# Kernel optimization log

Measured on AMD Instinct MI355X. Metric: run time of the kernel, lower is better.

## Reference

```python
import jax, jax.numpy as jnp
import numpy as np

EMBED_DIM = 384
NUM_HEADS = 6
HEAD_DIM = EMBED_DIM // NUM_HEADS
MLP_HIDDEN = 4 * EMBED_DIM
LN_EPS = 1e-5


def layer_norm(x, gamma, beta):
    mu = jnp.mean(x, axis=-1, keepdims=True)
    var = jnp.mean((x - mu) ** 2, axis=-1, keepdims=True)
    return (x - mu) * jax.lax.rsqrt(var + LN_EPS) * gamma + beta


def setup_inputs() -> dict:
    key = jax.random.key(0)
    ks = jax.random.split(key, 8)
    D, H = EMBED_DIM, MLP_HIDDEN
    s = 1.0 / np.sqrt(D)
    sh = 1.0 / np.sqrt(H)
    return {
        "x": jax.random.normal(ks[0], (16, 1024, D), dtype=jnp.float32),
        "ln1_g": jnp.ones((D,), jnp.float32),
        "ln1_b": jnp.zeros((D,), jnp.float32),
        "qkv_w": jax.random.uniform(ks[1], (3 * D, D), jnp.float32, -s, s),
        "qkv_b": jax.random.uniform(ks[2], (3 * D,), jnp.float32, -s, s),
        "proj_w": jax.random.uniform(ks[3], (D, D), jnp.float32, -s, s),
        "proj_b": jax.random.uniform(ks[4], (D,), jnp.float32, -s, s),
        "ln2_g": jnp.ones((D,), jnp.float32),
        "ln2_b": jnp.zeros((D,), jnp.float32),
        "fc1_w": jax.random.uniform(ks[5], (H, D), jnp.float32, -s, s),
        "fc1_b": jax.random.uniform(ks[6], (H,), jnp.float32, -s, s),
        "fc2_w": jax.random.uniform(ks[7], (D, H), jnp.float32, -sh, sh),
        "fc2_b": jnp.zeros((D,), jnp.float32),
    }


def reference(x, ln1_g, ln1_b, qkv_w, qkv_b, proj_w, proj_b,
              ln2_g, ln2_b, fc1_w, fc1_b, fc2_w, fc2_b):
    B, N, D = x.shape
    Hh, Dh = NUM_HEADS, HEAD_DIM
    scale = Dh ** -0.5

    # --- attention sublayer (pre-norm) ---
    h = layer_norm(x, ln1_g, ln1_b)
    qkv = h @ qkv_w.T + qkv_b                      # [B,N,3D]
    qkv = qkv.reshape(B, N, 3, Hh, Dh)
    q, k, v = (qkv[:, :, i].transpose(0, 2, 1, 3) for i in range(3))  # [B,H,N,Dh]
    attn = jax.nn.softmax(jnp.einsum('bhnd,bhmd->bhnm', q, k) * scale, axis=-1)
    o = jnp.einsum('bhnm,bhmd->bhnd', attn, v)     # [B,H,N,Dh]
    o = o.transpose(0, 2, 1, 3).reshape(B, N, D)
    x = x + (o @ proj_w.T + proj_b)

    # --- MLP sublayer (pre-norm) ---
    h = layer_norm(x, ln2_g, ln2_b)
    h = jax.nn.gelu(h @ fc1_w.T + fc1_b, approximate=False)
    x = x + (h @ fc2_w.T + fc2_b)
    return x
```

## Files before the change

kernel.cpp:

```cpp
#include <hip/hip_runtime.h>

typedef unsigned short u16;
typedef unsigned int   u32;
typedef __bf16  bf16x8 __attribute__((ext_vector_type(8)));
typedef __bf16  bf16x4_t __attribute__((ext_vector_type(4)));
typedef float   f32x4  __attribute__((ext_vector_type(4)));
typedef float   f32x2  __attribute__((ext_vector_type(2)));

struct Ptrs { const void* p[13]; };

extern "C" __device__ float __ocml_native_exp2_f32(float);

__device__ __forceinline__ float bf2f(u16 u) {
    union { unsigned int i; float f; } c; c.i = ((unsigned int)u) << 16; return c.f;
}
__device__ __forceinline__ u16 f2bf(float f) {
    union { float f; unsigned int i; } c; c.f = f;
    unsigned int u = c.i;
    unsigned int r = (u + 0x7fffu + ((u >> 16) & 1u)) >> 16;
    return (u16)r;
}

__device__ __forceinline__ float wave_sum(float x) {
#pragma unroll
    for (int m = 32; m >= 1; m >>= 1) x += __shfl_xor(x, m);
    return x;
}

__device__ __forceinline__ void g2l16(const u16* g, u16* l) {
    __builtin_amdgcn_global_load_lds(
        (__attribute__((address_space(1))) void*)g,
        (__attribute__((address_space(3))) void*)l, 16, 0, 0);
}

__device__ __forceinline__ int sniff_bf16(const u32* __restrict__ w) {
    int cnt = 0;
    for (int i = 0; i < 128; ++i) {
        u16 lo = (u16)(w[i] & 0xFFFFu);
        int e = (lo >> 7) & 0xFF;
        cnt += (e >= 117 && e <= 123) ? 1 : 0;
    }
    return (cnt >= 64) ? 1 : 0;
}

__global__ __launch_bounds__(256) void k_convert(Ptrs ps,
                                                 u16* __restrict__ cw,
                                                 int* __restrict__ flagp)
{
    const int cum[13] = {0,48,96,55392,55536,73968,74016,74064,74112,
                         147840,148032,221760,221808};
    const int off[12] = {0,384,768,443136,444288,591744,
                         592128,592512,592896,1182720,1184256,1774080};
    const int flag = sniff_bf16((const u32*)ps.p[3]);
    if (blockIdx.x == 0 && threadIdx.x == 0) *flagp = flag;
    int c = blockIdx.x * 256 + threadIdx.x;
    if (c >= 221808) return;
    int seg = 0;
#pragma unroll
    for (int i = 1; i < 12; ++i) seg += (c >= cum[i]) ? 1 : 0;
    int e = (c - cum[seg]) * 8;
    u16* dst = cw + off[seg] + e;
    if (flag) {
        *(uint4*)dst = *((const uint4*)ps.p[seg + 1] + (e >> 3));
    } else {
        const float* s = (const float*)ps.p[seg + 1] + e;
        u16 tmp[8];
#pragma unroll
        for (int t = 0; t < 8; ++t) tmp[t] = f2bf(s[t]);
        *(uint4*)dst = *(const uint4*)tmp;
    }
}

__global__ __launch_bounds__(256) void k_ln1cvt(const void* __restrict__ xin,
                                                const u16* __restrict__ g,
                                                const u16* __restrict__ b,
                                                u16* __restrict__ cx,
                                                u16* __restrict__ h,
                                                const int* __restrict__ flagp)
{
    const int wid = threadIdx.x >> 6, lane = threadIdx.x & 63;
    const int row = blockIdx.x * 4 + wid;
    const int e0 = lane * 6;
    float v[6]; u16 raw[6];
    if (*flagp) {
        const u16* p = (const u16*)xin + (size_t)row * 384 + e0;
        u32 w0 = *(const u32*)(p);
        u32 w1 = *(const u32*)(p + 2);
        u32 w2 = *(const u32*)(p + 4);
        raw[0] = (u16)w0; raw[1] = (u16)(w0 >> 16);
        raw[2] = (u16)w1; raw[3] = (u16)(w1 >> 16);
        raw[4] = (u16)w2; raw[5] = (u16)(w2 >> 16);
#pragma unroll
        for (int t = 0; t < 6; t++) v[t] = bf2f(raw[t]);
    } else {
        const float* p = (const float*)xin + (size_t)row * 384 + e0;
        f32x2 a0 = *(const f32x2*)(p);
        f32x2 a1 = *(const f32x2*)(p + 2);
        f32x2 a2 = *(const f32x2*)(p + 4);
        v[0] = a0[0]; v[1] = a0[1]; v[2] = a1[0];
        v[3] = a1[1]; v[4] = a2[0]; v[5] = a2[1];
#pragma unroll
        for (int t = 0; t < 6; t++) raw[t] = f2bf(v[t]);
    }
    u32* pc = (u32*)(cx + (size_t)row * 384 + e0);
    pc[0] = (u32)raw[0] | ((u32)raw[1] << 16);
    pc[1] = (u32)raw[2] | ((u32)raw[3] << 16);
    pc[2] = (u32)raw[4] | ((u32)raw[5] << 16);
    float s = 0.f;
#pragma unroll
    for (int t = 0; t < 6; t++) s += v[t];
    const float mu = wave_sum(s) * (1.0f / 384.0f);
    float vs = 0.f;
#pragma unroll
    for (int t = 0; t < 6; t++) { float d = v[t] - mu; vs += d * d; }
    const float var = wave_sum(vs) * (1.0f / 384.0f);
    const float rs = rsqrtf(var + 1e-5f);
    const u32* gg = (const u32*)(g + e0);
    const u32* bb = (const u32*)(b + e0);
    u32 gw[3] = {gg[0], gg[1], gg[2]};
    u32 bw[3] = {bb[0], bb[1], bb[2]};
    u16 ow[6];
#pragma unroll
    for (int t = 0; t < 6; t++) {
        u16 ge = (u16)(gw[t >> 1] >> ((t & 1) * 16));
        u16 be = (u16)(bw[t >> 1] >> ((t & 1) * 16));
        ow[t] = f2bf((v[t] - mu) * rs * bf2f(ge) + bf2f(be));
    }
    u32* po = (u32*)(h + (size_t)row * 384 + e0);
    po[0] = (u32)ow[0] | ((u32)ow[1] << 16);
    po[1] = (u32)ow[2] | ((u32)ow[3] << 16);
    po[2] = (u32)ow[4] | ((u32)ow[5] << 16);
}

__device__ __forceinline__ void gemm_core_128(const u16* __restrict__ A,
                                              const u16* __restrict__ B,
                                              int K, int m0, int n0,
                                              f32x4 (&acc)[4][4])
{
    __shared__ __align__(16) u16 As[128 * 64];
    __shared__ __align__(16) u16 Bs[128 * 64];

    const int tid  = threadIdx.x;
    const int lane = tid & 63;
    const int wid  = tid >> 6;
    const int wm  = (wid >> 1) * 64;
    const int wn  = (wid & 1) * 64;
    const int l15 = lane & 15;
    const int g   = lane >> 4;
    const int srow   = lane >> 3;
    const int schunk = ((lane & 7) ^ srow) * 8;

    const u16* Abase = A + (size_t)(m0 + wid * 32 + srow) * K + schunk;
    const u16* Bbase = B + (size_t)(n0 + wid * 32 + srow) * K + schunk;

    for (int kk = 0; kk < K; kk += 64) {
        __syncthreads();
#pragma unroll
        for (int t = 0; t < 4; ++t) {
            g2l16(Abase + (size_t)t * 8 * K + kk, &As[(wid * 32 + t * 8) * 64]);
            g2l16(Bbase + (size_t)t * 8 * K + kk, &Bs[(wid * 32 + t * 8) * 64]);
        }
        __syncthreads();

#pragma unroll
        for (int ks = 0; ks < 2; ++ks) {
            bf16x8 af[4], bfr[4];
#pragma unroll
            for (int i = 0; i < 4; i++) {
                int row = wm + 16 * i + l15;
                int p = ((ks * 4 + g) ^ (l15 & 7)) * 8;
                af[i] = __builtin_bit_cast(bf16x8,
                         *(const uint4*)&As[row * 64 + p]);
            }
#pragma unroll
            for (int j = 0; j < 4; j++) {
                int row = wn + 16 * j + l15;
                int p = ((ks * 4 + g) ^ (l15 & 7)) * 8;
                bfr[j] = __builtin_bit_cast(bf16x8,
                         *(const uint4*)&Bs[row * 64 + p]);
            }
#pragma unroll
            for (int i = 0; i < 4; i++)
#pragma unroll
                for (int j = 0; j < 4; j++)
                    acc[i][j] = __builtin_amdgcn_mfma_f32_16x16x32_bf16(
                                    af[i], bfr[j], acc[i][j], 0, 0, 0);
        }
    }
}

__device__ __forceinline__ void gemm_core_128x64(const u16* __restrict__ A,
                                                 const u16* __restrict__ B,
                                                 int K, int m0, int n0,
                                                 f32x4 (&acc)[4][2])
{
    __shared__ __align__(16) u16 As[128 * 64];
    __shared__ __align__(16) u16 Bs[64 * 64];

    const int tid  = threadIdx.x;
    const int lane = tid & 63;
    const int wid  = tid >> 6;
    const int wm  = (wid >> 1) * 64;
    const int wn  = (wid & 1) * 32;
    const int l15 = lane & 15;
    const int g   = lane >> 4;
    const int srow   = lane >> 3;
    const int schunk = ((lane & 7) ^ srow) * 8;

    const u16* Abase = A + (size_t)(m0 + wid * 32 + srow) * K + schunk;
    const u16* Bbase = B + (size_t)(n0 + wid * 16 + srow) * K + schunk;

    for (int kk = 0; kk < K; kk += 64) {
        __syncthreads();
#pragma unroll
        for (int t = 0; t < 4; ++t)
            g2l16(Abase + (size_t)t * 8 * K + kk, &As[(wid * 32 + t * 8) * 64]);
#pragma unroll
        for (int t = 0; t < 2; ++t)
            g2l16(Bbase + (size_t)t * 8 * K + kk, &Bs[(wid * 16 + t * 8) * 64]);
        __syncthreads();

#pragma unroll
        for (int ks = 0; ks < 2; ++ks) {
            bf16x8 af[4], bfr[2];
#pragma unroll
            for (int i = 0; i < 4; i++) {
                int row = wm + 16 * i + l15;
                int p = ((ks * 4 + g) ^ (l15 & 7)) * 8;
                af[i] = __builtin_bit_cast(bf16x8,
                         *(const uint4*)&As[row * 64 + p]);
            }
#pragma unroll
            for (int j = 0; j < 2; j++) {
                int row = wn + 16 * j + l15;
                int p = ((ks * 4 + g) ^ (l15 & 7)) * 8;
                bfr[j] = __builtin_bit_cast(bf16x8,
                         *(const uint4*)&Bs[row * 64 + p]);
            }
#pragma unroll
            for (int i = 0; i < 4; i++)
#pragma unroll
                for (int j = 0; j < 2; j++)
                    acc[i][j] = __builtin_amdgcn_mfma_f32_16x16x32_bf16(
                                    af[i], bfr[j], acc[i][j], 0, 0, 0);
        }
    }
}

__global__ __launch_bounds__(256) void k_layernorm(const u16* __restrict__ in,
                                                   const u16* __restrict__ g,
                                                   const u16* __restrict__ b,
                                                   u16* __restrict__ out,
                                                   int nrows)
{
    const int wid = threadIdx.x >> 6, lane = threadIdx.x & 63;
    const int row = blockIdx.x * 4 + wid;
    if (row >= nrows) return;
    const int e0 = lane * 6;
    float v[6];
    const u16* p = in + (size_t)row * 384 + e0;
    u32 w0 = *(const u32*)(p);
    u32 w1 = *(const u32*)(p + 2);
    u32 w2 = *(const u32*)(p + 4);
    v[0] = bf2f((u16)w0); v[1] = bf2f((u16)(w0 >> 16));
    v[2] = bf2f((u16)w1); v[3] = bf2f((u16)(w1 >> 16));
    v[4] = bf2f((u16)w2); v[5] = bf2f((u16)(w2 >> 16));
    float s = 0.f;
#pragma unroll
    for (int t = 0; t < 6; t++) s += v[t];
    const float mu = wave_sum(s) * (1.0f / 384.0f);
    float vs = 0.f;
#pragma unroll
    for (int t = 0; t < 6; t++) { float d = v[t] - mu; vs += d * d; }
    const float var = wave_sum(vs) * (1.0f / 384.0f);
    const float rs = rsqrtf(var + 1e-5f);
    const u32* gg = (const u32*)(g + e0);
    const u32* bb = (const u32*)(b + e0);
    u32 gw[3] = {gg[0], gg[1], gg[2]};
    u32 bw[3] = {bb[0], bb[1], bb[2]};
    u16 ow[6];
#pragma unroll
    for (int t = 0; t < 6; t++) {
        u16 ge = (u16)(gw[t >> 1] >> ((t & 1) * 16));
        u16 be = (u16)(bw[t >> 1] >> ((t & 1) * 16));
        ow[t] = f2bf((v[t] - mu) * rs * bf2f(ge) + bf2f(be));
    }
    u32* po = (u32*)(out + (size_t)row * 384 + e0);
    po[0] = (u32)ow[0] | ((u32)ow[1] << 16);
    po[1] = (u32)ow[2] | ((u32)ow[3] << 16);
    po[2] = (u32)ow[4] | ((u32)ow[5] << 16);
}

__global__ __launch_bounds__(256) void k_gemm_qkv(const u16* __restrict__ A,
                                                  const u16* __restrict__ W,
                                                  const u16* __restrict__ bias,
                                                  u16* __restrict__ q,
                                                  u16* __restrict__ kbuf,
                                                  u16* __restrict__ vT)
{
    const int id = blockIdx.x, slot = id & 7, idx = id >> 3;
    const int m0 = (slot * 16 + idx / 9) * 128;
    const int n0 = (idx % 9) * 128;
    f32x4 acc[4][4];
#pragma unroll
    for (int i = 0; i < 4; i++)
#pragma unroll
        for (int j = 0; j < 4; j++) acc[i][j] = f32x4{0.f, 0.f, 0.f, 0.f};
    gemm_core_128(A, W, 384, m0, n0, acc);
    const int lane = threadIdx.x & 63, wid = threadIdx.x >> 6;
    const int wm = (wid >> 1) * 64, wn = (wid & 1) * 64;
    const int l15 = lane & 15, rq = (lane >> 4) * 4;
#pragma unroll
    for (int i = 0; i < 4; i++) {
        const int grb = m0 + wm + 16 * i + rq;
        const int bb = grb >> 10, nn = grb & 1023;
#pragma unroll
        for (int j = 0; j < 4; j++) {
            const int gc = n0 + wn + 16 * j + l15;
            const int part = gc / 384, rem = gc % 384;
            const int head = rem >> 6, dh = rem & 63;
            const int bh = bb * 6 + head;
            float vals[4];
#pragma unroll
            for (int r = 0; r < 4; r++) vals[r] = acc[i][j][r] + bf2f(bias[gc]);
            if (part == 2) {
                u32 lo = (u32)f2bf(vals[0]) | ((u32)f2bf(vals[1]) << 16);
                u32 hi = (u32)f2bf(vals[2]) | ((u32)f2bf(vals[3]) << 16);
                uint2 pk; pk.x = lo; pk.y = hi;
                *(uint2*)&vT[((size_t)bh * 64 + dh) * 1024 + nn] = pk;
            } else {
                u16* dst = part ? kbuf : q;
#pragma unroll
                for (int r = 0; r < 4; r++)
                    dst[((size_t)bh * 1024 + nn + r) * 64 + dh] = f2bf(vals[r]);
            }
        }
    }
}

__global__ __launch_bounds__(256) void k_attn(const u16* __restrict__ q,
                                              const u16* __restrict__ kk,
                                              const u16* __restrict__ vT,
                                              u16* __restrict__ o)
{
    __shared__ __align__(16) u16 Ks[128 * 64];
    __shared__ __align__(16) u16 Vs[2][64 * 64];
    __shared__ __align__(16) u16 Ps[128 * 64];

    const int tid = threadIdx.x, lane = tid & 63, wid = tid >> 6;
    const int l15 = lane & 15, g = lane >> 4, q8 = g * 8;
    const int id = blockIdx.x;
    const int bh = (id & 7) * 12 + ((id >> 3) >> 3);
    const int q0 = ((id >> 3) & 7) * 128;
    const int wrow = wid * 32;

    const u16* Q = q  + (size_t)bh * 65536;
    const u16* K = kk + (size_t)bh * 65536;
    const u16* V = vT + (size_t)bh * 65536;

    const int srow   = lane >> 3;
    const int schunk = ((lane & 7) ^ srow) * 8;
    const int rd0 = ((0 + g) ^ (l15 & 7)) * 8;
    const int rd1 = ((4 + g) ^ (l15 & 7)) * 8;
    int pcol[4];
#pragma unroll
    for (int ip = 0; ip < 4; ++ip)
        pcol[ip] = (((ip * 2 + (g >> 1)) ^ (l15 & 7)) * 8) + (g & 1) * 4;

    bf16x8 aq[2][2];
#pragma unroll
    for (int jp = 0; jp < 2; ++jp)
#pragma unroll
        for (int ks = 0; ks < 2; ++ks) {
            bf16x8 t = __builtin_bit_cast(bf16x8,
                *(const uint4*)&Q[(size_t)(q0 + wrow + jp * 16 + l15) * 64
                                  + ks * 32 + q8]);
#pragma unroll
            for (int e = 0; e < 8; ++e)
                t[e] = (__bf16)((float)t[e] * 0.18033688f);
            aq[jp][ks] = t;
        }

    f32x4 ob[2][4];
#pragma unroll
    for (int i = 0; i < 2; ++i)
#pragma unroll
        for (int j = 0; j < 4; ++j) ob[i][j] = f32x4{0.f, 0.f, 0.f, 0.f};
    float lsum[2] = {0.f, 0.f};

    for (int kt2 = 0; kt2 < 8; ++kt2) {
        __syncthreads();
#pragma unroll
        for (int t = 0; t < 4; ++t) {
            int r0 = wid * 32 + t * 8;
            g2l16(&K[(size_t)(kt2 * 128 + r0 + srow) * 64 + schunk], &Ks[r0 * 64]);
        }
#pragma unroll
        for (int h = 0; h < 2; ++h)
#pragma unroll
            for (int t = 0; t < 2; ++t) {
                int r0 = wid * 16 + t * 8;
                g2l16(&V[(size_t)(r0 + srow) * 1024 + kt2 * 128 + h * 64 + schunk],
                      &Vs[h][r0 * 64]);
            }
        __syncthreads();

#pragma unroll 1
        for (int h = 0; h < 2; ++h) {
            f32x4 st[4][2];
#pragma unroll
            for (int ip = 0; ip < 4; ++ip)
#pragma unroll
                for (int jp = 0; jp < 2; ++jp) st[ip][jp] = f32x4{0.f,0.f,0.f,0.f};
            __builtin_amdgcn_s_setprio(1);
#pragma unroll
            for (int ip = 0; ip < 4; ++ip) {
                int rbase = (h * 64 + ip * 16 + l15) * 64;
                bf16x8 bk0 = __builtin_bit_cast(bf16x8,
                    *(const uint4*)&Ks[rbase + rd0]);
                bf16x8 bk1 = __builtin_bit_cast(bf16x8,
                    *(const uint4*)&Ks[rbase + rd1]);
#pragma unroll
                for (int jp = 0; jp < 2; ++jp) {
                    st[ip][jp] = __builtin_amdgcn_mfma_f32_16x16x32_bf16(
                                    bk0, aq[jp][0], st[ip][jp], 0, 0, 0);
                    st[ip][jp] = __builtin_amdgcn_mfma_f32_16x16x32_bf16(
                                    bk1, aq[jp][1], st[ip][jp], 0, 0, 0);
                }
            }
            __builtin_amdgcn_s_setprio(0);

#pragma unroll
            for (int jp = 0; jp < 2; ++jp) {
                float ps = 0.f;
#pragma unroll
                for (int ip = 0; ip < 4; ++ip)
#pragma unroll
                    for (int r = 0; r < 4; ++r) {
                        float p = __ocml_native_exp2_f32(st[ip][jp][r]);
                        st[ip][jp][r] = p;
                        ps += p;
                    }
                lsum[jp] += ps;
            }

#pragma unroll
            for (int ip = 0; ip < 4; ++ip)
#pragma unroll
                for (int jp = 0; jp < 2; ++jp) {
                    bf16x4_t pk;
#pragma unroll
                    for (int r = 0; r < 4; ++r) pk[r] = (__bf16)st[ip][jp][r];
                    *(bf16x4_t*)&Ps[(wrow + jp*16 + l15) * 64 + pcol[ip]] = pk;
                }

            __builtin_amdgcn_s_setprio(1);
#pragma unroll
            for (int ks = 0; ks < 2; ++ks) {
                const int rdo = ks ? rd1 : rd0;
                bf16x8 ap[2];
#pragma unroll
                for (int i = 0; i < 2; ++i)
                    ap[i] = __builtin_bit_cast(bf16x8,
                        *(const uint4*)&Ps[(wrow + i*16 + l15) * 64 + rdo]);
#pragma unroll
                for (int jv = 0; jv < 4; ++jv) {
                    bf16x8 bv = __builtin_bit_cast(bf16x8,
                        *(const uint4*)&Vs[h][(jv * 16 + l15) * 64 + rdo]);
#pragma unroll
                    for (int i = 0; i < 2; ++i)
                        ob[i][jv] = __builtin_amdgcn_mfma_f32_16x16x32_bf16(
                                      ap[i], bv, ob[i][jv], 0, 0, 0);
                }
            }
            __builtin_amdgcn_s_setprio(0);
        }
    }

#pragma unroll
    for (int jp = 0; jp < 2; ++jp) {
        lsum[jp] += __shfl_xor(lsum[jp], 16);
        lsum[jp] += __shfl_xor(lsum[jp], 32);
    }
    const int bb = bh / 6, hh = bh % 6;
#pragma unroll
    for (int i = 0; i < 2; ++i)
#pragma unroll
        for (int r = 0; r < 4; ++r) {
            int src = (lane & 48) | (g * 4 + r);
            float linv = 1.0f / __shfl(lsum[i], src);
            int row = q0 + wrow + i * 16 + g * 4 + r;
#pragma unroll
            for (int jv = 0; jv < 4; ++jv) {
                int dh = jv * 16 + l15;
                o[((size_t)(bb * 1024 + row)) * 384 + hh * 64 + dh] =
                    f2bf(ob[i][jv][r] * linv);
            }
        }
}

__global__ __launch_bounds__(256) void k_gemm_proj(const u16* __restrict__ A,
                                                   const u16* __restrict__ W,
                                                   const u16* __restrict__ bias,
                                                   const u16* __restrict__ xin,
                                                   u16* __restrict__ x1)
{
    const int id = blockIdx.x, slot = id & 7, idx = id >> 3;
    const int m0 = (slot * 16 + idx / 6) * 128;
    const int n0 = (idx % 6) * 64;
    f32x4 acc[4][2];
#pragma unroll
    for (int i = 0; i < 4; i++)
#pragma unroll
        for (int j = 0; j < 2; j++) acc[i][j] = f32x4{0.f, 0.f, 0.f, 0.f};
    gemm_core_128x64(A, W, 384, m0, n0, acc);
    const int lane = threadIdx.x & 63, wid = threadIdx.x >> 6;
    const int wm = (wid >> 1) * 64, wn = (wid & 1) * 32;
    const int l15 = lane & 15, rq = (lane >> 4) * 4;
#pragma unroll
    for (int i = 0; i < 4; i++)
#pragma unroll
        for (int j = 0; j < 2; j++)
#pragma unroll
            for (int r = 0; r < 4; r++) {
                int gr = m0 + wm + 16 * i + rq + r;
                int gc = n0 + wn + 16 * j + l15;
                size_t ix = (size_t)gr * 384 + gc;
                x1[ix] = f2bf(acc[i][j][r] + bf2f(bias[gc]) + bf2f(xin[ix]));
            }
}

__global__ __launch_bounds__(256) void k_gemm_fc1(const u16* __restrict__ A,
                                                  const u16* __restrict__ W,
                                                  const u16* __restrict__ bias,
                                                  u16* __restrict__ hmid)
{
    const int id = blockIdx.x, slot = id & 7, idx = id >> 3;
    const int mbase = (slot * 8 + idx / 12) * 256;
    const int n0 = (idx % 12) * 128;
#pragma unroll 1
    for (int sub = 0; sub < 2; ++sub) {
        const int m0 = mbase + sub * 128;
        f32x4 acc[4][4];
#pragma unroll
        for (int i = 0; i < 4; i++)
#pragma unroll
            for (int j = 0; j < 4; j++) acc[i][j] = f32x4{0.f, 0.f, 0.f, 0.f};
        gemm_core_128(A, W, 384, m0, n0, acc);
        const int lane = threadIdx.x & 63, wid = threadIdx.x >> 6;
        const int wm = (wid >> 1) * 64, wn = (wid & 1) * 64;
        const int l15 = lane & 15, rq = (lane >> 4) * 4;
#pragma unroll
        for (int i = 0; i < 4; i++)
#pragma unroll
            for (int j = 0; j < 4; j++)
#pragma unroll
                for (int r = 0; r < 4; r++) {
                    int gr = m0 + wm + 16 * i + rq + r;
                    int gc = n0 + wn + 16 * j + l15;
                    float v = acc[i][j][r] + bf2f(bias[gc]);
                    float u = v * (1.5957691f + 0.0713548f * v * v);
                    float ge = v * __builtin_amdgcn_rcpf(1.0f + __expf(-u));
                    hmid[(size_t)gr * 1536 + gc] = f2bf(ge);
                }
    }
}

__global__ __launch_bounds__(256) void k_gemm_fc2(const u16* __restrict__ A,
                                                  const u16* __restrict__ W,
                                                  const u16* __restrict__ bias,
                                                  const u16* __restrict__ x1,
                                                  void* __restrict__ outv,
                                                  const int* __restrict__ flagp)
{
    const int id = blockIdx.x, slot = id & 7, idx = id >> 3;
    const int m0 = (slot * 16 + idx / 6) * 128;
    const int n0 = (idx % 6) * 64;
    f32x4 acc[4][2];
#pragma unroll
    for (int i = 0; i < 4; i++)
#pragma unroll
        for (int j = 0; j < 2; j++) acc[i][j] = f32x4{0.f, 0.f, 0.f, 0.f};
    gemm_core_128x64(A, W, 1536, m0, n0, acc);
    const int lane = threadIdx.x & 63, wid = threadIdx.x >> 6;
    const int wm = (wid >> 1) * 64, wn = (wid & 1) * 32;
    const int l15 = lane & 15, rq = (lane >> 4) * 4;
    const int isbf = *flagp;
    u16*   ob = (u16*)outv;
    float* of = (float*)outv;
#pragma unroll
    for (int i = 0; i < 4; i++)
#pragma unroll
        for (int j = 0; j < 2; j++)
#pragma unroll
            for (int r = 0; r < 4; r++) {
                int gr = m0 + wm + 16 * i + rq + r;
                int gc = n0 + wn + 16 * j + l15;
                size_t ix = (size_t)gr * 384 + gc;
                float v = acc[i][j][r] + bf2f(bias[gc]) + bf2f(x1[ix]);
                if (isbf) ob[ix] = f2bf(v);
                else      of[ix] = v;
            }
}

extern "C" void kernel_launch(void* const* d_in, const int* in_sizes, int n_in,
                              void* d_out, int out_size, void* d_ws, size_t ws_size,
                              hipStream_t stream)
{
    char* ws = (char*)d_ws;
    u16*   cw   = (u16*)(ws + 0);
    int*   flag = (int*)(ws + 3548928);
    u16*   cx   = (u16*)(ws + 3549184);
    u16*   h    = (u16*)(ws + 16132096);
    u16*   x1   = (u16*)(ws + 28715008);
    u16*   q    = (u16*)(ws + 53880832);
    u16*   kbuf = (u16*)(ws + 66463744);
    u16*   vT   = (u16*)(ws + 79046656);
    u16*   o    = (u16*)(ws + 91629568);
    u16*   hmid = (u16*)(ws + 53880832);

    const u16* c_ln1_g  = cw + 0;
    const u16* c_ln1_b  = cw + 384;
    const u16* c_qkv_w  = cw + 768;
    const u16* c_qkv_b  = cw + 443136;
    const u16* c_proj_w = cw + 444288;
    const u16* c_proj_b = cw + 591744;
    const u16* c_ln2_g  = cw + 592128;
    const u16* c_ln2_b  = cw + 592512;
    const u16* c_fc1_w  = cw + 592896;
    const u16* c_fc1_b  = cw + 1182720;
    const u16* c_fc2_w  = cw + 1184256;
    const u16* c_fc2_b  = cw + 1774080;

    Ptrs ps;
    for (int i = 0; i < 13; ++i) ps.p[i] = d_in[i];

    k_convert<<<867, 256, 0, stream>>>(ps, cw, flag);
    k_ln1cvt<<<4096, 256, 0, stream>>>(d_in[0], c_ln1_g, c_ln1_b, cx, h, flag);
    k_gemm_qkv<<<1152, 256, 0, stream>>>(h, c_qkv_w, c_qkv_b, q, kbuf, vT);
    k_attn<<<768, 256, 0, stream>>>(q, kbuf, vT, o);
    k_gemm_proj<<<768, 256, 0, stream>>>(o, c_proj_w, c_proj_b, cx, x1);
    k_layernorm<<<4096, 256, 0, stream>>>(x1, c_ln2_g, c_ln2_b, h, 16384);
    k_gemm_fc1<<<768, 256, 0, stream>>>(h, c_fc1_w, c_fc1_b, hmid);
    k_gemm_fc2<<<768, 256, 0, stream>>>(hmid, c_fc2_w, c_fc2_b, x1,
                                        d_out, flag);
    (void)in_sizes; (void)n_in; (void)out_size; (void)ws_size; (void)c_fc2_b;
}
```

Before: 268.2 us.

## Fuse weight conversion with LN1, swap QKV MFMA operands, use exp2 GELU

Merges the weight-conversion kernel and the LN1/convert kernel into one launch, with the LN1 blocks reading gamma and beta straight from the original inputs. The bf16 sniff loop is cut from 128 to 32 samples. The QKV GEMM swaps its MFMA operands so each lane holds consecutive head-dim values, which lets q and k be written as packed 8-byte stores while vT now gets scalar stores. The GELU epilogue folds the log2(e) factor into its constants and calls native exp2. Together these aim to remove one launch and cut store and transcendental overhead, at the cost of uncoalesced vT writes and a less robust dtype sniff.

```diff
diff --git a/kernel.cpp b/kernel.cpp
--- a/kernel.cpp
+++ b/kernel.cpp
@@ -35,55 +35,54 @@
 
 __device__ __forceinline__ int sniff_bf16(const u32* __restrict__ w) {
     int cnt = 0;
-    for (int i = 0; i < 128; ++i) {
+    for (int i = 0; i < 32; ++i) {
         u16 lo = (u16)(w[i] & 0xFFFFu);
         int e = (lo >> 7) & 0xFF;
         cnt += (e >= 117 && e <= 123) ? 1 : 0;
     }
-    return (cnt >= 64) ? 1 : 0;
-}
-
-__global__ __launch_bounds__(256) void k_convert(Ptrs ps,
+    return (cnt >= 16) ? 1 : 0;
+}
+
+__global__ __launch_bounds__(256) void k_cvt_ln1(Ptrs ps,
                                                  u16* __restrict__ cw,
-                                                 int* __restrict__ flagp)
-{
-    const int cum[13] = {0,48,96,55392,55536,73968,74016,74064,74112,
-                         147840,148032,221760,221808};
-    const int off[12] = {0,384,768,443136,444288,591744,
-                         592128,592512,592896,1182720,1184256,1774080};
+                                                 int* __restrict__ flagp,
+                                                 u16* __restrict__ cx,
+                                                 u16* __restrict__ h)
+{
     const int flag = sniff_bf16((const u32*)ps.p[3]);
     if (blockIdx.x == 0 && threadIdx.x == 0) *flagp = flag;
-    int c = blockIdx.x * 256 + threadIdx.x;
-    if (c >= 221808) return;
-    int seg = 0;
-#pragma unroll
-    for (int i = 1; i < 12; ++i) seg += (c >= cum[i]) ? 1 : 0;
-    int e = (c - cum[seg]) * 8;
-    u16* dst = cw + off[seg] + e;
-    if (flag) {
-        *(uint4*)dst = *((const uint4*)ps.p[seg + 1] + (e >> 3));
-    } else {
-        const float* s = (const float*)ps.p[seg + 1] + e;
-        u16 tmp[8];
-#pragma unroll
-        for (int t = 0; t < 8; ++t) tmp[t] = f2bf(s[t]);
-        *(uint4*)dst = *(const uint4*)tmp;
-    }
-}
-
-__global__ __launch_bounds__(256) void k_ln1cvt(const void* __restrict__ xin,
-                                                const u16* __restrict__ g,
-                                                const u16* __restrict__ b,
-                                                u16* __restrict__ cx,
-                                                u16* __restrict__ h,
-                                                const int* __restrict__ flagp)
-{
+
+    if (blockIdx.x < 867) {
+        const int cum[13] = {0,48,96,55392,55536,73968,74016,74064,74112,
+                             147840,148032,221760,221808};
+        const int off[12] = {0,384,768,443136,444288,591744,
+                             592128,592512,592896,1182720,1184256,1774080};
+        int c = blockIdx.x * 256 + threadIdx.x;
+        if (c >= 221808) return;
+        int seg = 0;
+#pragma unroll
+        for (int i = 1; i < 12; ++i) seg += (c >= cum[i]) ? 1 : 0;
+        int e = (c - cum[seg]) * 8;
+        u16* dst = cw + off[seg] + e;
+        if (flag) {
+            *(uint4*)dst = *((const uint4*)ps.p[seg + 1] + (e >> 3));
+        } else {
+            const float* s = (const float*)ps.p[seg + 1] + e;
+            u16 tmp[8];
+#pragma unroll
+            for (int t = 0; t < 8; ++t) tmp[t] = f2bf(s[t]);
+            *(uint4*)dst = *(const uint4*)tmp;
+        }
+        return;
+    }
+
     const int wid = threadIdx.x >> 6, lane = threadIdx.x & 63;
-    const int row = blockIdx.x * 4 + wid;
+    const int row = (blockIdx.x - 867) * 4 + wid;
     const int e0 = lane * 6;
     float v[6]; u16 raw[6];
-    if (*flagp) {
-        const u16* p = (const u16*)xin + (size_t)row * 384 + e0;
+    float gv[6], bv[6];
+    if (flag) {
+        const u16* p = (const u16*)ps.p[0] + (size_t)row * 384 + e0;
         u32 w0 = *(const u32*)(p);
         u32 w1 = *(const u32*)(p + 2);
         u32 w2 = *(const u32*)(p + 4);
@@ -92,8 +91,12 @@
         raw[4] = (u16)w2; raw[5] = (u16)(w2 >> 16);
 #pragma unroll
         for (int t = 0; t < 6; t++) v[t] = bf2f(raw[t]);
+        const u16* gp = (const u16*)ps.p[1] + e0;
+        const u16* bp = (const u16*)ps.p[2] + e0;
+#pragma unroll
+        for (int t = 0; t < 6; t++) { gv[t] = bf2f(gp[t]); bv[t] = bf2f(bp[t]); }
     } else {
-        const float* p = (const float*)xin + (size_t)row * 384 + e0;
+        const float* p = (const float*)ps.p[0] + (size_t)row * 384 + e0;
         f32x2 a0 = *(const f32x2*)(p);
         f32x2 a1 = *(const f32x2*)(p + 2);
         f32x2 a2 = *(const f32x2*)(p + 4);
@@ -101,6 +104,10 @@
         v[3] = a1[1]; v[4] = a2[0]; v[5] = a2[1];
 #pragma unroll
         for (int t = 0; t < 6; t++) raw[t] = f2bf(v[t]);
+        const float* gp = (const float*)ps.p[1] + e0;
+        const float* bp = (const float*)ps.p[2] + e0;
+#pragma unroll
+        for (int t = 0; t < 6; t++) { gv[t] = gp[t]; bv[t] = bp[t]; }
     }
     u32* pc = (u32*)(cx + (size_t)row * 384 + e0);
     pc[0] = (u32)raw[0] | ((u32)raw[1] << 16);
@@ -115,23 +122,17 @@
     for (int t = 0; t < 6; t++) { float d = v[t] - mu; vs += d * d; }
     const float var = wave_sum(vs) * (1.0f / 384.0f);
     const float rs = rsqrtf(var + 1e-5f);
-    const u32* gg = (const u32*)(g + e0);
-    const u32* bb = (const u32*)(b + e0);
-    u32 gw[3] = {gg[0], gg[1], gg[2]};
-    u32 bw[3] = {bb[0], bb[1], bb[2]};
     u16 ow[6];
 #pragma unroll
-    for (int t = 0; t < 6; t++) {
-        u16 ge = (u16)(gw[t >> 1] >> ((t & 1) * 16));
-        u16 be = (u16)(bw[t >> 1] >> ((t & 1) * 16));
-        ow[t] = f2bf((v[t] - mu) * rs * bf2f(ge) + bf2f(be));
-    }
+    for (int t = 0; t < 6; t++)
+        ow[t] = f2bf((v[t] - mu) * rs * gv[t] + bv[t]);
     u32* po = (u32*)(h + (size_t)row * 384 + e0);
     po[0] = (u32)ow[0] | ((u32)ow[1] << 16);
     po[1] = (u32)ow[2] | ((u32)ow[3] << 16);
     po[2] = (u32)ow[4] | ((u32)ow[5] << 16);
 }
 
+template <bool SWAP = false>
 __device__ __forceinline__ void gemm_core_128(const u16* __restrict__ A,
                                               const u16* __restrict__ B,
                                               int K, int m0, int n0,
@@ -182,9 +183,14 @@
 #pragma unroll
             for (int i = 0; i < 4; i++)
 #pragma unroll
-                for (int j = 0; j < 4; j++)
-                    acc[i][j] = __builtin_amdgcn_mfma_f32_16x16x32_bf16(
-                                    af[i], bfr[j], acc[i][j], 0, 0, 0);
+                for (int j = 0; j < 4; j++) {
+                    if (SWAP)
+                        acc[i][j] = __builtin_amdgcn_mfma_f32_16x16x32_bf16(
+                                        bfr[j], af[i], acc[i][j], 0, 0, 0);
+                    else
+                        acc[i][j] = __builtin_amdgcn_mfma_f32_16x16x32_bf16(
+                                        af[i], bfr[j], acc[i][j], 0, 0, 0);
+                }
         }
     }
 }
@@ -306,33 +312,33 @@
     for (int i = 0; i < 4; i++)
 #pragma unroll
         for (int j = 0; j < 4; j++) acc[i][j] = f32x4{0.f, 0.f, 0.f, 0.f};
-    gemm_core_128(A, W, 384, m0, n0, acc);
+    gemm_core_128<true>(A, W, 384, m0, n0, acc);
     const int lane = threadIdx.x & 63, wid = threadIdx.x >> 6;
     const int wm = (wid >> 1) * 64, wn = (wid & 1) * 64;
     const int l15 = lane & 15, rq = (lane >> 4) * 4;
 #pragma unroll
     for (int i = 0; i < 4; i++) {
-        const int grb = m0 + wm + 16 * i + rq;
-        const int bb = grb >> 10, nn = grb & 1023;
+        const int gr = m0 + wm + 16 * i + l15;
+        const int bb = gr >> 10, nn = gr & 1023;
 #pragma unroll
         for (int j = 0; j < 4; j++) {
-            const int gc = n0 + wn + 16 * j + l15;
-            const int part = gc / 384, rem = gc % 384;
-            const int head = rem >> 6, dh = rem & 63;
+            const int gcb = n0 + wn + 16 * j + rq;
+            const int part = gcb / 384, rem = gcb % 384;
+            const int head = rem >> 6, dhb = rem & 63;
             const int bh = bb * 6 + head;
             float vals[4];
 #pragma unroll
-            for (int r = 0; r < 4; r++) vals[r] = acc[i][j][r] + bf2f(bias[gc]);
+            for (int r = 0; r < 4; r++) vals[r] = acc[i][j][r] + bf2f(bias[gcb + r]);
             if (part == 2) {
+#pragma unroll
+                for (int r = 0; r < 4; r++)
+                    vT[((size_t)bh * 64 + dhb + r) * 1024 + nn] = f2bf(vals[r]);
+            } else {
+                u16* dst = part ? kbuf : q;
                 u32 lo = (u32)f2bf(vals[0]) | ((u32)f2bf(vals[1]) << 16);
                 u32 hi = (u32)f2bf(vals[2]) | ((u32)f2bf(vals[3]) << 16);
                 uint2 pk; pk.x = lo; pk.y = hi;
-                *(uint2*)&vT[((size_t)bh * 64 + dh) * 1024 + nn] = pk;
-            } else {
-                u16* dst = part ? kbuf : q;
-#pragma unroll
-                for (int r = 0; r < 4; r++)
-                    dst[((size_t)bh * 1024 + nn + r) * 64 + dh] = f2bf(vals[r]);
+                *(uint2*)&dst[((size_t)bh * 1024 + nn) * 64 + dhb] = pk;
             }
         }
     }
@@ -559,8 +565,9 @@
                     int gr = m0 + wm + 16 * i + rq + r;
                     int gc = n0 + wn + 16 * j + l15;
                     float v = acc[i][j][r] + bf2f(bias[gc]);
-                    float u = v * (1.5957691f + 0.0713548f * v * v);
-                    float ge = v * __builtin_amdgcn_rcpf(1.0f + __expf(-u));
+                    float u2 = v * (2.3022084f + 0.1029433f * v * v);
+                    float ge = v * __builtin_amdgcn_rcpf(
+                                   1.0f + __ocml_native_exp2_f32(-u2));
                     hmid[(size_t)gr * 1536 + gc] = f2bf(ge);
                 }
     }
@@ -619,8 +626,6 @@
     u16*   o    = (u16*)(ws + 91629568);
     u16*   hmid = (u16*)(ws + 53880832);
 
-    const u16* c_ln1_g  = cw + 0;
-    const u16* c_ln1_b  = cw + 384;
     const u16* c_qkv_w  = cw + 768;
     const u16* c_qkv_b  = cw + 443136;
     const u16* c_proj_w = cw + 444288;
@@ -635,8 +640,7 @@
     Ptrs ps;
     for (int i = 0; i < 13; ++i) ps.p[i] = d_in[i];
 
-    k_convert<<<867, 256, 0, stream>>>(ps, cw, flag);
-    k_ln1cvt<<<4096, 256, 0, stream>>>(d_in[0], c_ln1_g, c_ln1_b, cx, h, flag);
+    k_cvt_ln1<<<4963, 256, 0, stream>>>(ps, cw, flag, cx, h);
     k_gemm_qkv<<<1152, 256, 0, stream>>>(h, c_qkv_w, c_qkv_b, q, kbuf, vT);
     k_attn<<<768, 256, 0, stream>>>(q, kbuf, vT, o);
     k_gemm_proj<<<768, 256, 0, stream>>>(o, c_proj_w, c_proj_b, cx, x1);
```

After: 259.9 us (median of 2 runs). -3.1%, faster.
